# Optimization experiments

Hardware: AMD Instinct MI355X
Metric: run time of the kernel (lower is better)

## Reference

```python
import jax, jax.numpy as jnp
import numpy as np

N = 50000      # nodes
E = 800000     # edges (avg degree 16)
B = 128        # graphs in batch
F_IN = 30      # raw node feature dim
PORT_DIM = 32
FLAG_DIM = 2
H = 64         # hidden_dim; also F_IN+PORT_DIM+FLAG_DIM = 64
L = 3          # number of GraphConv layers
C = 10         # num_classes
TOTAL_PORTS = 65536
TCP_FLAGS_VALUES = 256


def setup_inputs() -> dict:
    key = jax.random.key(0)
    ks = jax.random.split(key, 20)
    s = 0.1  # weight init scale
    return {
        "x": jax.random.normal(ks[0], (N, F_IN), jnp.float32),
        "dst_ports": jax.random.randint(ks[1], (N,), 0, TOTAL_PORTS, jnp.int64),
        "tcp_flags": jax.random.randint(ks[2], (N,), 0, TCP_FLAGS_VALUES, jnp.int64),
        "edge_index": jax.random.randint(ks[3], (2, E), 0, N, jnp.int64),
        "batch": jnp.sort(jax.random.randint(ks[4], (N,), 0, B, jnp.int64)),
        # learned parameters
        "emb_port": jax.random.normal(ks[5], (TOTAL_PORTS, PORT_DIM), jnp.float32) * s,
        "emb_flags": jax.random.normal(ks[6], (TCP_FLAGS_VALUES, FLAG_DIM), jnp.float32) * s,
        "Wrel": jax.random.normal(ks[7], (L, H, H), jnp.float32) * s,   # lin_rel weight (out,in)
        "brel": jax.random.normal(ks[8], (L, H), jnp.float32) * s,      # lin_rel bias
        "Wroot": jax.random.normal(ks[9], (L, H, H), jnp.float32) * s,  # lin_root weight, no bias
        "fc1_W": jax.random.normal(ks[10], (H, H), jnp.float32) * s,
        "fc1_b": jax.random.normal(ks[11], (H,), jnp.float32) * s,
        "fc2_W": jax.random.normal(ks[12], (H, H), jnp.float32) * s,
        "fc2_b": jax.random.normal(ks[13], (H,), jnp.float32) * s,
        "fc3_W": jax.random.normal(ks[14], (C, H), jnp.float32) * s,
        "fc3_b": jax.random.normal(ks[15], (C,), jnp.float32) * s,
    }


def reference(x, dst_ports, tcp_flags, edge_index, batch,
              emb_port, emb_flags, Wrel, brel, Wroot,
              fc1_W, fc1_b, fc2_W, fc2_b, fc3_W, fc3_b):
    # embedding lookups + concat -> [N, 64]
    h = jnp.concatenate([x, emb_port[dst_ports], emb_flags[tcp_flags]], axis=1)
    src, dst = edge_index[0], edge_index[1]
    # PyG GraphConv (aggr='add'): h' = lin_rel(sum_{j->i} h_j) + lin_root(h_i)
    for l in range(L):
        agg = jax.ops.segment_sum(h[src], dst, num_segments=N)  # gather + scatter-add
        h = agg @ Wrel[l].T + brel[l] + h @ Wroot[l].T
        h = jax.nn.relu(h)  # dropout inactive (eval mode)
    # global_max_pool over graphs -> [B, H]
    g = jax.ops.segment_max(h, batch, num_segments=B)
    # MLP head (dropout inactive)
    g = jax.nn.relu(g @ fc1_W.T + fc1_b)
    g = jax.nn.relu(g @ fc2_W.T + fc2_b)
    return g @ fc3_W.T + fc3_b
```

## Files before the change

### kernel.cpp

```cpp
#include <hip/hip_runtime.h>

#define NN 50000
#define NE 800000
#define NB 128
#define FIN 30
#define H 64
#define NC 10
#define L 3

#define EBS 2048
#define NEB 391
#define NBX 391
#define NS (NBX * NEB)
#define SECAP 2816

typedef unsigned int uint;
typedef unsigned short ushort;
typedef __attribute__((ext_vector_type(8))) short bf16x8;
typedef __attribute__((ext_vector_type(4))) float f32x4;

__device__ __forceinline__ ushort f2bf(float x) {
    uint u = __float_as_uint(x);
    u += 0x7fffu + ((u >> 16) & 1u);
    return (ushort)(u >> 16);
}
__device__ __forceinline__ float bf_lo(uint v) { return __uint_as_float(v << 16); }
__device__ __forceinline__ float bf_hi(uint v) { return __uint_as_float(v & 0xffff0000u); }


__global__ __launch_bounds__(256) void prep_weights_kernel(
    const float* __restrict__ Wrel, const float* __restrict__ Wroot,
    ushort* __restrict__ Wb)
{
    int t = blockIdx.x * 256 + threadIdx.x;
    if (t >= L * 2 * H * H) return;
    int l = t / (2 * H * H), rem = t % (2 * H * H);
    int mat = rem / (H * H), jk = rem % (H * H);
    const float* W = mat ? Wroot : Wrel;
    Wb[t] = f2bf(W[l * H * H + jk]);
}

__global__ __launch_bounds__(256) void count_kernel(
    const int* __restrict__ dst, int* __restrict__ counts)
{
    __shared__ int cnt[NBX];
    int eb = blockIdx.x, tid = threadIdx.x;
    for (int t = tid; t < NBX; t += 256) cnt[t] = 0;
    __syncthreads();
#pragma unroll
    for (int q = 0; q < 8; ++q) {
        int e = eb * EBS + q * 256 + tid;
        if (e < NE) atomicAdd(&cnt[dst[e] >> 7], 1);
    }
    __syncthreads();
    for (int t = tid; t < NBX; t += 256) counts[t * NEB + eb] = cnt[t];
}

__global__ __launch_bounds__(1024) void scanA1_kernel(
    const int* __restrict__ counts, int* __restrict__ offs, int* __restrict__ bsum)
{
    __shared__ int wsum[16];
    int i = blockIdx.x * 1024 + threadIdx.x;
    int lane = threadIdx.x & 63;
    int wv = threadIdx.x >> 6;
    int v = (i < NS) ? counts[i] : 0;
    int s = v;
    for (int off = 1; off < 64; off <<= 1) {
        int t = __shfl_up(s, off);
        if (lane >= off) s += t;
    }
    if (lane == 63) wsum[wv] = s;
    __syncthreads();
    if (wv == 0) {
        int ws = (lane < 16) ? wsum[lane] : 0;
        for (int off = 1; off < 16; off <<= 1) {
            int t = __shfl_up(ws, off);
            if (lane >= off) ws += t;
        }
        if (lane < 16) wsum[lane] = ws;
    }
    __syncthreads();
    int base = (wv > 0) ? wsum[wv - 1] : 0;
    s += base;
    if (i < NS) offs[i] = s - v;
    if (threadIdx.x == 1023) bsum[blockIdx.x] = s;
}

__global__ __launch_bounds__(256) void scanA2_kernel(int* __restrict__ bsum, int nblk)
{
    __shared__ int arr[256];
    int t = threadIdx.x;
    int v = (t < nblk) ? bsum[t] : 0;
    arr[t] = v;
    __syncthreads();
    for (int off = 1; off < 256; off <<= 1) {
        int u = (t >= off) ? arr[t - off] : 0;
        __syncthreads();
        arr[t] += u;
        __syncthreads();
    }
    if (t < nblk) bsum[t] = arr[t] - v;
}

__global__ __launch_bounds__(1024) void scanA3_kernel(
    int* __restrict__ offs, const int* __restrict__ bsum)
{
    int b = blockIdx.x + 1;
    int i = b * 1024 + threadIdx.x;
    if (i < NS) offs[i] += bsum[b];
}

__global__ __launch_bounds__(256) void scatter_ranked_kernel(
    const int* __restrict__ src, const int* __restrict__ dst,
    const int* __restrict__ offs, int* __restrict__ tmp)
{
    __shared__ int cur[NBX];
    int eb = blockIdx.x, tid = threadIdx.x;
    for (int t = tid; t < NBX; t += 256) cur[t] = offs[t * NEB + eb];
    __syncthreads();
#pragma unroll
    for (int q = 0; q < 8; ++q) {
        int e = eb * EBS + q * 256 + tid;
        if (e < NE) {
            int d = dst[e];
            int b = d >> 7;
            int pos = atomicAdd(&cur[b], 1);
            tmp[pos] = (src[e] << 7) | (d & 127);
        }
    }
}

__global__ __launch_bounds__(256) void bucket_sort_kernel(
    const int* __restrict__ tmp, const int* __restrict__ offs,
    int* __restrict__ edge_arr, int2* __restrict__ node_range)
{
    __shared__ int se[SECAP];
    __shared__ int cnt[128];
    __shared__ int off[128];
    __shared__ int cur[128];
    int b = blockIdx.x, tid = threadIdx.x;
    int start = offs[b * NEB];
    int end   = (b + 1 < NBX) ? offs[(b + 1) * NEB] : NE;
    int ec = end - start; if (ec > SECAP) ec = SECAP;

    if (tid < 128) cnt[tid] = 0;
    __syncthreads();
    for (int t = tid; t < ec; t += 256) {
        int v = tmp[start + t];
        se[t] = v;
        atomicAdd(&cnt[v & 127], 1);
    }
    __syncthreads();
    if (tid < 64) {
        int v0 = cnt[2 * tid], v1 = cnt[2 * tid + 1];
        int s = v0 + v1;
        for (int o = 1; o < 64; o <<= 1) {
            int t = __shfl_up(s, o);
            if (tid >= o) s += t;
        }
        off[2 * tid]     = s - v1 - v0;
        off[2 * tid + 1] = s - v1;
        cur[2 * tid]     = s - v1 - v0;
        cur[2 * tid + 1] = s - v1;
    }
    __syncthreads();
    for (int t = tid; t < ec; t += 256) {
        int v = se[t];
        int p = atomicAdd(&cur[v & 127], 1);
        edge_arr[start + p] = v & ~127;
    }
    if (tid < 128) {
        int n = b * 128 + tid;
        if (n < NN) node_range[n] = make_int2(start + off[tid], cnt[tid]);
    }
}

__global__ __launch_bounds__(256) void gemm0_fused_kernel(
    const float* __restrict__ x, const int* __restrict__ ports,
    const int* __restrict__ flags, const float* __restrict__ emb_port,
    const float* __restrict__ emb_flags,
    const ushort* __restrict__ Wb, const float* __restrict__ brel,
    ushort* __restrict__ z0, ushort* __restrict__ z1)
{
    __shared__ float sf[64 * 65];
    __shared__ float so[64 * 65];
    int tid = threadIdx.x, lane = tid & 63, w = tid >> 6;
    int node0 = blockIdx.x * 64;

    for (int t = tid; t < 4096; t += 256) {
        int r = t >> 6, f = t & 63;
        int n = node0 + r;
        float v = 0.f;
        if (n < NN) {
            if (f < FIN)       v = x[(size_t)n * FIN + f];
            else if (f < 62)   v = emb_port[(size_t)ports[n] * 32 + (f - FIN)];
            else               v = emb_flags[(size_t)flags[n] * 2 + (f - 62)];
        }
        sf[r * 65 + f] = v;
    }
    __syncthreads();

    int m  = lane & 15;
    int kg = lane >> 4;
    int rloc = w * 16 + m;
    const float* fr = &sf[rloc * 65 + kg * 8];
    bf16x8 a0, a1;
#pragma unroll
    for (int i = 0; i < 8; ++i) {
        a0[i] = (short)f2bf(fr[i]);
        a1[i] = (short)f2bf(fr[32 + i]);
    }

    f32x4 acc0[4], acc1[4];
#pragma unroll
    for (int jt = 0; jt < 4; ++jt) {
        const ushort* wr0 = Wb + ((size_t)(jt * 16 + m)) * 64 + kg * 8;
        const ushort* wr1 = wr0 + (size_t)H * H;
        bf16x8 b00 = *(const bf16x8*)(wr0);
        bf16x8 b01 = *(const bf16x8*)(wr0 + 32);
        bf16x8 b10 = *(const bf16x8*)(wr1);
        bf16x8 b11 = *(const bf16x8*)(wr1 + 32);
        float bias = brel[jt * 16 + m];
        acc0[jt] = f32x4{0.f, 0.f, 0.f, 0.f};
        acc1[jt] = f32x4{bias, bias, bias, bias};
        acc0[jt] = __builtin_amdgcn_mfma_f32_16x16x32_bf16(a0, b00, acc0[jt], 0, 0, 0);
        acc0[jt] = __builtin_amdgcn_mfma_f32_16x16x32_bf16(a1, b01, acc0[jt], 0, 0, 0);
        acc1[jt] = __builtin_amdgcn_mfma_f32_16x16x32_bf16(a0, b10, acc1[jt], 0, 0, 0);
        acc1[jt] = __builtin_amdgcn_mfma_f32_16x16x32_bf16(a1, b11, acc1[jt], 0, 0, 0);
    }

    int nl = w * 16 + kg * 4;

#pragma unroll
    for (int jt = 0; jt < 4; ++jt)
#pragma unroll
        for (int r = 0; r < 4; ++r)
            so[(nl + r) * 65 + jt * 16 + m] = acc0[jt][r];
    __syncthreads();
    for (int t = tid; t < 512; t += 256) {
        int rr = t >> 3, oct = t & 7;
        if (node0 + rr < NN) {
            const float* s = &so[rr * 65 + oct * 8];
            uint4 v;
            v.x = (uint)f2bf(s[0]) | ((uint)f2bf(s[1]) << 16);
            v.y = (uint)f2bf(s[2]) | ((uint)f2bf(s[3]) << 16);
            v.z = (uint)f2bf(s[4]) | ((uint)f2bf(s[5]) << 16);
            v.w = (uint)f2bf(s[6]) | ((uint)f2bf(s[7]) << 16);
            *((uint4*)(z0 + (size_t)node0 * H) + t) = v;
        }
    }
    __syncthreads();

#pragma unroll
    for (int jt = 0; jt < 4; ++jt)
#pragma unroll
        for (int r = 0; r < 4; ++r)
            so[(nl + r) * 65 + jt * 16 + m] = acc1[jt][r];
    __syncthreads();
    for (int t = tid; t < 512; t += 256) {
        int rr = t >> 3, oct = t & 7;
        if (node0 + rr < NN) {
            const float* s = &so[rr * 65 + oct * 8];
            uint4 v;
            v.x = (uint)f2bf(s[0]) | ((uint)f2bf(s[1]) << 16);
            v.y = (uint)f2bf(s[2]) | ((uint)f2bf(s[3]) << 16);
            v.z = (uint)f2bf(s[4]) | ((uint)f2bf(s[5]) << 16);
            v.w = (uint)f2bf(s[6]) | ((uint)f2bf(s[7]) << 16);
            *((uint4*)(z1 + (size_t)node0 * H) + t) = v;
        }
    }
}

__global__ __launch_bounds__(256) void gemm_kernel(
    const ushort* __restrict__ h_in, const ushort* __restrict__ Wb,
    const float* __restrict__ brel,
    ushort* __restrict__ z0, ushort* __restrict__ z1)
{
    __shared__ float so[64 * 65];
    int tid = threadIdx.x, lane = tid & 63, w = tid >> 6;
    int m  = lane & 15;
    int kg = lane >> 4;
    int node0 = blockIdx.x * 64 + w * 16;

    int row = node0 + m; if (row >= NN) row = NN - 1;
    const ushort* hr = h_in + (size_t)row * H + kg * 8;
    bf16x8 a0 = *(const bf16x8*)(hr);
    bf16x8 a1 = *(const bf16x8*)(hr + 32);

    f32x4 acc0[4], acc1[4];
#pragma unroll
    for (int jt = 0; jt < 4; ++jt) {
        const ushort* wr0 = Wb + ((size_t)(jt * 16 + m)) * 64 + kg * 8;
        const ushort* wr1 = wr0 + (size_t)H * H;
        bf16x8 b00 = *(const bf16x8*)(wr0);
        bf16x8 b01 = *(const bf16x8*)(wr0 + 32);
        bf16x8 b10 = *(const bf16x8*)(wr1);
        bf16x8 b11 = *(const bf16x8*)(wr1 + 32);
        float bias = brel[jt * 16 + m];
        acc0[jt] = f32x4{0.f, 0.f, 0.f, 0.f};
        acc1[jt] = f32x4{bias, bias, bias, bias};
        acc0[jt] = __builtin_amdgcn_mfma_f32_16x16x32_bf16(a0, b00, acc0[jt], 0, 0, 0);
        acc0[jt] = __builtin_amdgcn_mfma_f32_16x16x32_bf16(a1, b01, acc0[jt], 0, 0, 0);
        acc1[jt] = __builtin_amdgcn_mfma_f32_16x16x32_bf16(a0, b10, acc1[jt], 0, 0, 0);
        acc1[jt] = __builtin_amdgcn_mfma_f32_16x16x32_bf16(a1, b11, acc1[jt], 0, 0, 0);
    }

    int nl = w * 16 + kg * 4;
    int nodeS0 = blockIdx.x * 64;

#pragma unroll
    for (int jt = 0; jt < 4; ++jt)
#pragma unroll
        for (int r = 0; r < 4; ++r)
            so[(nl + r) * 65 + jt * 16 + m] = acc0[jt][r];
    __syncthreads();
    for (int t = tid; t < 512; t += 256) {
        int rr = t >> 3, oct = t & 7;
        if (nodeS0 + rr < NN) {
            const float* s = &so[rr * 65 + oct * 8];
            uint4 v;
            v.x = (uint)f2bf(s[0]) | ((uint)f2bf(s[1]) << 16);
            v.y = (uint)f2bf(s[2]) | ((uint)f2bf(s[3]) << 16);
            v.z = (uint)f2bf(s[4]) | ((uint)f2bf(s[5]) << 16);
            v.w = (uint)f2bf(s[6]) | ((uint)f2bf(s[7]) << 16);
            *((uint4*)(z0 + (size_t)nodeS0 * H) + t) = v;
        }
    }
    __syncthreads();

#pragma unroll
    for (int jt = 0; jt < 4; ++jt)
#pragma unroll
        for (int r = 0; r < 4; ++r)
            so[(nl + r) * 65 + jt * 16 + m] = acc1[jt][r];
    __syncthreads();
    for (int t = tid; t < 512; t += 256) {
        int rr = t >> 3, oct = t & 7;
        if (nodeS0 + rr < NN) {
            const float* s = &so[rr * 65 + oct * 8];
            uint4 v;
            v.x = (uint)f2bf(s[0]) | ((uint)f2bf(s[1]) << 16);
            v.y = (uint)f2bf(s[2]) | ((uint)f2bf(s[3]) << 16);
            v.z = (uint)f2bf(s[4]) | ((uint)f2bf(s[5]) << 16);
            v.w = (uint)f2bf(s[6]) | ((uint)f2bf(s[7]) << 16);
            *((uint4*)(z1 + (size_t)nodeS0 * H) + t) = v;
        }
    }
}

__global__ __launch_bounds__(256) void gather_relu_kernel(
    const ushort* __restrict__ z0, const ushort* __restrict__ z1,
    const int2* __restrict__ node_range, const int* __restrict__ edge_arr,
    ushort* __restrict__ h_out)
{
    int tid = blockIdx.x * 256 + threadIdx.x;
    int n = tid >> 3, oct = tid & 7;
    if (n >= NN) return;
    int2 rng = node_range[n];
    int p0 = rng.x, p1 = rng.x + rng.y;
    const char* zb = (const char*)z0 + oct * 16;
    float a[8] = {0.f,0.f,0.f,0.f,0.f,0.f,0.f,0.f};
    for (int p = p0; p < p1; p += 8) {
        bool g[8]; int o[8]; uint4 v[8];
#pragma unroll
        for (int q = 0; q < 8; ++q) {
            g[q] = (p + q) < p1;
            o[q] = g[q] ? edge_arr[p + q] : 0;
        }
#pragma unroll
        for (int q = 0; q < 8; ++q) {
            v[q] = make_uint4(0u, 0u, 0u, 0u);
            if (g[q]) v[q] = *(const uint4*)(zb + o[q]);
        }
#pragma unroll
        for (int q = 0; q < 8; ++q) {
            a[0] += bf_lo(v[q].x); a[1] += bf_hi(v[q].x);
            a[2] += bf_lo(v[q].y); a[3] += bf_hi(v[q].y);
            a[4] += bf_lo(v[q].z); a[5] += bf_hi(v[q].z);
            a[6] += bf_lo(v[q].w); a[7] += bf_hi(v[q].w);
        }
    }
    uint4 sv = *(const uint4*)((const char*)z1 + (size_t)n * 128 + oct * 16);
    a[0] += bf_lo(sv.x); a[1] += bf_hi(sv.x);
    a[2] += bf_lo(sv.y); a[3] += bf_hi(sv.y);
    a[4] += bf_lo(sv.z); a[5] += bf_hi(sv.z);
    a[6] += bf_lo(sv.w); a[7] += bf_hi(sv.w);
    uint4 o;
    o.x = (uint)f2bf(fmaxf(a[0], 0.f)) | ((uint)f2bf(fmaxf(a[1], 0.f)) << 16);
    o.y = (uint)f2bf(fmaxf(a[2], 0.f)) | ((uint)f2bf(fmaxf(a[3], 0.f)) << 16);
    o.z = (uint)f2bf(fmaxf(a[4], 0.f)) | ((uint)f2bf(fmaxf(a[5], 0.f)) << 16);
    o.w = (uint)f2bf(fmaxf(a[6], 0.f)) | ((uint)f2bf(fmaxf(a[7], 0.f)) << 16);
    *((uint4*)h_out + tid) = o;
}

__global__ __launch_bounds__(256) void pool_mlp_kernel(
    const ushort* __restrict__ h, const int* __restrict__ batch,
    const float* __restrict__ fc1W, const float* __restrict__ fc1b,
    const float* __restrict__ fc2W, const float* __restrict__ fc2b,
    const float* __restrict__ fc3W, const float* __restrict__ fc3b,
    float* __restrict__ out)
{
    __shared__ float red[4][64];
    __shared__ float s0[64];
    __shared__ float s1[64];
    __shared__ float s2[64];
    int b = blockIdx.x;
    int tid = threadIdx.x;
    int f = tid & 63, w = tid >> 6;
    int lo = 0, hi = NN;
    while (lo < hi) { int mid = (lo + hi) >> 1; if (batch[mid] < b) lo = mid + 1; else hi = mid; }
    int lo2 = lo, hi2 = NN;
    while (lo2 < hi2) { int mid = (lo2 + hi2) >> 1; if (batch[mid] < b + 1) lo2 = mid + 1; else hi2 = mid; }
    float m = -3.402823466e38f;
    for (int n = lo + w; n < lo2; n += 4) {
        ushort u = h[(size_t)n * H + f];
        m = fmaxf(m, __uint_as_float((uint)u << 16));
    }
    red[w][f] = m;
    __syncthreads();
    int j = tid;
    if (tid < 64)
        s0[j] = fmaxf(fmaxf(red[0][j], red[1][j]), fmaxf(red[2][j], red[3][j]));
    __syncthreads();
    float acc = 0.f;
    if (tid < 64) {
        acc = fc1b[j];
        for (int k = 0; k < 64; ++k) acc = fmaf(s0[k], fc1W[j * 64 + k], acc);
    }
    __syncthreads();
    if (tid < 64) s1[j] = fmaxf(acc, 0.f);
    __syncthreads();
    if (tid < 64) {
        acc = fc2b[j];
        for (int k = 0; k < 64; ++k) acc = fmaf(s1[k], fc2W[j * 64 + k], acc);
    }
    __syncthreads();
    if (tid < 64) s2[j] = fmaxf(acc, 0.f);
    __syncthreads();
    if (tid < NC) {
        acc = fc3b[j];
        for (int k = 0; k < 64; ++k) acc = fmaf(s2[k], fc3W[j * 64 + k], acc);
        out[b * NC + j] = acc;
    }
}


extern "C" void kernel_launch(void* const* d_in, const int* in_sizes, int n_in,
                              void* d_out, int out_size, void* d_ws, size_t ws_size,
                              hipStream_t stream)
{
    const float* x         = (const float*)d_in[0];
    const int*   dst_ports = (const int*)d_in[1];
    const int*   tcp_flags = (const int*)d_in[2];
    const int*   edge_src_in = (const int*)d_in[3];
    const int*   edge_dst_in = edge_src_in + NE;
    const int*   batch     = (const int*)d_in[4];
    const float* emb_port  = (const float*)d_in[5];
    const float* emb_flags = (const float*)d_in[6];
    const float* Wrel      = (const float*)d_in[7];
    const float* brel      = (const float*)d_in[8];
    const float* Wroot     = (const float*)d_in[9];
    const float* fc1W      = (const float*)d_in[10];
    const float* fc1b      = (const float*)d_in[11];
    const float* fc2W      = (const float*)d_in[12];
    const float* fc2b      = (const float*)d_in[13];
    const float* fc3W      = (const float*)d_in[14];
    const float* fc3b      = (const float*)d_in[15];
    float* out = (float*)d_out;

    char* ws = (char*)d_ws;
    size_t off = 0;
    auto alloc = [&](size_t bytes) {
        void* p = ws + off;
        off += (bytes + 255) & ~(size_t)255;
        return p;
    };
    ushort* hA        = (ushort*)alloc((size_t)NN * H * 2);
    ushort* hB        = (ushort*)alloc((size_t)NN * H * 2);
    ushort* z0        = (ushort*)alloc((size_t)NN * H * 2);
    ushort* z1        = (ushort*)alloc((size_t)NN * H * 2);
    int*    counts    = (int*)alloc((size_t)NS * 4);
    int*    tmp       = (int*)alloc((size_t)NE * 4);
    int*    edge_arr  = (int*)alloc((size_t)NE * 4);
    int2*   node_range= (int2*)alloc((size_t)NN * 8);
    int*    bsum      = (int*)alloc((size_t)256 * 4);
    ushort* Wb        = (ushort*)alloc((size_t)L * 2 * H * H * 2);

    const int SBLK = (NS + 1023) / 1024;

    prep_weights_kernel<<<96, 256, 0, stream>>>(Wrel, Wroot, Wb);

    count_kernel<<<NEB, 256, 0, stream>>>(edge_dst_in, counts);
    scanA1_kernel<<<SBLK, 1024, 0, stream>>>(counts, counts, bsum);
    scanA2_kernel<<<1, 256, 0, stream>>>(bsum, SBLK);
    scanA3_kernel<<<SBLK - 1, 1024, 0, stream>>>(counts, bsum);
    scatter_ranked_kernel<<<NEB, 256, 0, stream>>>(edge_src_in, edge_dst_in, counts, tmp);
    bucket_sort_kernel<<<NBX, 256, 0, stream>>>(tmp, counts, edge_arr, node_range);

    const int ggrid = (NN + 63) / 64;
    const int agrid = (NN * 8 + 255) / 256;
    gemm0_fused_kernel<<<ggrid, 256, 0, stream>>>(
        x, dst_ports, tcp_flags, emb_port, emb_flags, Wb, brel, z0, z1);
    gather_relu_kernel<<<agrid, 256, 0, stream>>>(z0, z1, node_range, edge_arr, hA);

    gemm_kernel<<<ggrid, 256, 0, stream>>>(
        hA, Wb + (size_t)1 * 2 * H * H, brel + 1 * H, z0, z1);
    gather_relu_kernel<<<agrid, 256, 0, stream>>>(z0, z1, node_range, edge_arr, hB);
    gemm_kernel<<<ggrid, 256, 0, stream>>>(
        hB, Wb + (size_t)2 * 2 * H * H, brel + 2 * H, z0, z1);
    gather_relu_kernel<<<agrid, 256, 0, stream>>>(z0, z1, node_range, edge_arr, hA);

    pool_mlp_kernel<<<NB, 256, 0, stream>>>(
        hA, batch, fc1W, fc1b, fc2W, fc2b, fc3W, fc3b, out);
}
```

Measured before the change: 272.3 us.

## Merge setup kernels, pad edge lists to remove gather guards, widen pooling

Folds weight conversion into the count kernel and the edge scatter into the first GEMM launch, so fewer kernels launch and independent work shares one grid. Per-node edge lists are padded to multiples of eight with a pointer to a zeroed sentinel row, which lets the gather loop drop its bounds checks. Pooling now uses 512 threads per graph. The padding adds edge array memory and extra sentinel loads, and the fused launches rely on block-index splitting.

New measurement: 243.2 us. -10.7%, faster.

```diff
diff --git a/kernel.cpp b/kernel.cpp
--- a/kernel.cpp
+++ b/kernel.cpp
@@ -13,6 +13,8 @@
 #define NBX 391
 #define NS (NBX * NEB)
 #define SECAP 2816
+#define PCAP 3456
+#define ZOFF (NN << 7)
 
 typedef unsigned int uint;
 typedef unsigned short ushort;
@@ -28,32 +30,34 @@
 __device__ __forceinline__ float bf_hi(uint v) { return __uint_as_float(v & 0xffff0000u); }
 
 
-__global__ __launch_bounds__(256) void prep_weights_kernel(
+__global__ __launch_bounds__(256) void count_prep_kernel(
+    const int* __restrict__ dst, int* __restrict__ counts,
     const float* __restrict__ Wrel, const float* __restrict__ Wroot,
-    ushort* __restrict__ Wb)
-{
-    int t = blockIdx.x * 256 + threadIdx.x;
-    if (t >= L * 2 * H * H) return;
-    int l = t / (2 * H * H), rem = t % (2 * H * H);
-    int mat = rem / (H * H), jk = rem % (H * H);
-    const float* W = mat ? Wroot : Wrel;
-    Wb[t] = f2bf(W[l * H * H + jk]);
-}
-
-__global__ __launch_bounds__(256) void count_kernel(
-    const int* __restrict__ dst, int* __restrict__ counts)
+    ushort* __restrict__ Wb, ushort* __restrict__ z0)
 {
     __shared__ int cnt[NBX];
-    int eb = blockIdx.x, tid = threadIdx.x;
-    for (int t = tid; t < NBX; t += 256) cnt[t] = 0;
-    __syncthreads();
-#pragma unroll
-    for (int q = 0; q < 8; ++q) {
-        int e = eb * EBS + q * 256 + tid;
-        if (e < NE) atomicAdd(&cnt[dst[e] >> 7], 1);
-    }
-    __syncthreads();
-    for (int t = tid; t < NBX; t += 256) counts[t * NEB + eb] = cnt[t];
+    int bid = blockIdx.x, tid = threadIdx.x;
+    if (bid < NEB) {
+        for (int t = tid; t < NBX; t += 256) cnt[t] = 0;
+        __syncthreads();
+#pragma unroll
+        for (int q = 0; q < 8; ++q) {
+            int e = bid * EBS + q * 256 + tid;
+            if (e < NE) atomicAdd(&cnt[dst[e] >> 7], 1);
+        }
+        __syncthreads();
+        for (int t = tid; t < NBX; t += 256) counts[t * NEB + bid] = cnt[t];
+    } else if (bid < NEB + 96) {
+        int t = (bid - NEB) * 256 + tid;
+        if (t < L * 2 * H * H) {
+            int l = t / (2 * H * H), rem = t % (2 * H * H);
+            int mat = rem / (H * H), jk = rem % (H * H);
+            const float* W = mat ? Wroot : Wrel;
+            Wb[t] = f2bf(W[l * H * H + jk]);
+        }
+    } else {
+        if (tid < 8) ((uint4*)(z0 + (size_t)NN * H))[tid] = make_uint4(0u, 0u, 0u, 0u);
+    }
 }
 
 __global__ __launch_bounds__(1024) void scanA1_kernel(
@@ -110,72 +114,9 @@
     if (i < NS) offs[i] += bsum[b];
 }
 
-__global__ __launch_bounds__(256) void scatter_ranked_kernel(
-    const int* __restrict__ src, const int* __restrict__ dst,
-    const int* __restrict__ offs, int* __restrict__ tmp)
-{
-    __shared__ int cur[NBX];
-    int eb = blockIdx.x, tid = threadIdx.x;
-    for (int t = tid; t < NBX; t += 256) cur[t] = offs[t * NEB + eb];
-    __syncthreads();
-#pragma unroll
-    for (int q = 0; q < 8; ++q) {
-        int e = eb * EBS + q * 256 + tid;
-        if (e < NE) {
-            int d = dst[e];
-            int b = d >> 7;
-            int pos = atomicAdd(&cur[b], 1);
-            tmp[pos] = (src[e] << 7) | (d & 127);
-        }
-    }
-}
-
-__global__ __launch_bounds__(256) void bucket_sort_kernel(
-    const int* __restrict__ tmp, const int* __restrict__ offs,
-    int* __restrict__ edge_arr, int2* __restrict__ node_range)
-{
-    __shared__ int se[SECAP];
-    __shared__ int cnt[128];
-    __shared__ int off[128];
-    __shared__ int cur[128];
-    int b = blockIdx.x, tid = threadIdx.x;
-    int start = offs[b * NEB];
-    int end   = (b + 1 < NBX) ? offs[(b + 1) * NEB] : NE;
-    int ec = end - start; if (ec > SECAP) ec = SECAP;
-
-    if (tid < 128) cnt[tid] = 0;
-    __syncthreads();
-    for (int t = tid; t < ec; t += 256) {
-        int v = tmp[start + t];
-        se[t] = v;
-        atomicAdd(&cnt[v & 127], 1);
-    }
-    __syncthreads();
-    if (tid < 64) {
-        int v0 = cnt[2 * tid], v1 = cnt[2 * tid + 1];
-        int s = v0 + v1;
-        for (int o = 1; o < 64; o <<= 1) {
-            int t = __shfl_up(s, o);
-            if (tid >= o) s += t;
-        }
-        off[2 * tid]     = s - v1 - v0;
-        off[2 * tid + 1] = s - v1;
-        cur[2 * tid]     = s - v1 - v0;
-        cur[2 * tid + 1] = s - v1;
-    }
-    __syncthreads();
-    for (int t = tid; t < ec; t += 256) {
-        int v = se[t];
-        int p = atomicAdd(&cur[v & 127], 1);
-        edge_arr[start + p] = v & ~127;
-    }
-    if (tid < 128) {
-        int n = b * 128 + tid;
-        if (n < NN) node_range[n] = make_int2(start + off[tid], cnt[tid]);
-    }
-}
-
-__global__ __launch_bounds__(256) void gemm0_fused_kernel(
+__global__ __launch_bounds__(256) void scatter_gemm0_kernel(
+    const int* __restrict__ srcv, const int* __restrict__ dstv,
+    const int* __restrict__ offs, int* __restrict__ tmp,
     const float* __restrict__ x, const int* __restrict__ ports,
     const int* __restrict__ flags, const float* __restrict__ emb_port,
     const float* __restrict__ emb_flags,
@@ -184,8 +125,28 @@
 {
     __shared__ float sf[64 * 65];
     __shared__ float so[64 * 65];
-    int tid = threadIdx.x, lane = tid & 63, w = tid >> 6;
-    int node0 = blockIdx.x * 64;
+    __shared__ int cur[NBX];
+    int bid = blockIdx.x, tid = threadIdx.x;
+
+    if (bid < NEB) {
+        for (int t = tid; t < NBX; t += 256) cur[t] = offs[t * NEB + bid];
+        __syncthreads();
+#pragma unroll
+        for (int q = 0; q < 8; ++q) {
+            int e = bid * EBS + q * 256 + tid;
+            if (e < NE) {
+                int d = dstv[e];
+                int b = d >> 7;
+                int pos = atomicAdd(&cur[b], 1);
+                tmp[pos] = (srcv[e] << 7) | (d & 127);
+            }
+        }
+        return;
+    }
+
+    int gb = bid - NEB;
+    int lane = tid & 63, w = tid >> 6;
+    int node0 = gb * 64;
 
     for (int t = tid; t < 4096; t += 256) {
         int r = t >> 6, f = t & 63;
@@ -271,6 +232,58 @@
     }
 }
 
+__global__ __launch_bounds__(256) void bucket_sort_kernel(
+    const int* __restrict__ tmp, const int* __restrict__ offs,
+    int* __restrict__ edge_arr, int2* __restrict__ node_range)
+{
+    __shared__ int se[SECAP];
+    __shared__ int cnt[128];
+    __shared__ int po[128];
+    __shared__ int cur[128];
+    int b = blockIdx.x, tid = threadIdx.x;
+    int start = offs[b * NEB];
+    int end   = (b + 1 < NBX) ? offs[(b + 1) * NEB] : NE;
+    int ec = end - start; if (ec > SECAP) ec = SECAP;
+
+    if (tid < 128) cnt[tid] = 0;
+    __syncthreads();
+    for (int t = tid; t < ec; t += 256) {
+        int v = tmp[start + t];
+        se[t] = v;
+        atomicAdd(&cnt[v & 127], 1);
+    }
+    __syncthreads();
+    if (tid < 64) {
+        int c0 = cnt[2 * tid], c1 = cnt[2 * tid + 1];
+        int p0 = (c0 + 7) & ~7, p1 = (c1 + 7) & ~7;
+        int s = p0 + p1;
+        for (int o = 1; o < 64; o <<= 1) {
+            int t = __shfl_up(s, o);
+            if (tid >= o) s += t;
+        }
+        po[2 * tid]     = s - p1 - p0;
+        po[2 * tid + 1] = s - p1;
+        cur[2 * tid]     = s - p1 - p0;
+        cur[2 * tid + 1] = s - p1;
+    }
+    __syncthreads();
+    int base = b * PCAP;
+    for (int t = tid; t < ec; t += 256) {
+        int v = se[t];
+        int p = atomicAdd(&cur[v & 127], 1);
+        edge_arr[base + p] = v & ~127;
+    }
+    __syncthreads();
+    if (tid < 128) {
+        int c = cnt[tid];
+        int pd = (c + 7) & ~7;
+        for (int q = c; q < pd; ++q)
+            edge_arr[base + po[tid] + q] = ZOFF;
+        int n = b * 128 + tid;
+        if (n < NN) node_range[n] = make_int2(base + po[tid], c);
+    }
+}
+
 __global__ __launch_bounds__(256) void gemm_kernel(
     const ushort* __restrict__ h_in, const ushort* __restrict__ Wb,
     const float* __restrict__ brel,
@@ -357,20 +370,16 @@
     int n = tid >> 3, oct = tid & 7;
     if (n >= NN) return;
     int2 rng = node_range[n];
-    int p0 = rng.x, p1 = rng.x + rng.y;
+    int p0 = rng.x;
+    int pend = p0 + ((rng.y + 7) & ~7);
     const char* zb = (const char*)z0 + oct * 16;
     float a[8] = {0.f,0.f,0.f,0.f,0.f,0.f,0.f,0.f};
-    for (int p = p0; p < p1; p += 8) {
-        bool g[8]; int o[8]; uint4 v[8];
+    for (int p = p0; p < pend; p += 8) {
+        uint4 v[8];
 #pragma unroll
         for (int q = 0; q < 8; ++q) {
-            g[q] = (p + q) < p1;
-            o[q] = g[q] ? edge_arr[p + q] : 0;
-        }
-#pragma unroll
-        for (int q = 0; q < 8; ++q) {
-            v[q] = make_uint4(0u, 0u, 0u, 0u);
-            if (g[q]) v[q] = *(const uint4*)(zb + o[q]);
+            int o = edge_arr[p + q];
+            v[q] = *(const uint4*)(zb + o);
         }
 #pragma unroll
         for (int q = 0; q < 8; ++q) {
@@ -393,14 +402,14 @@
     *((uint4*)h_out + tid) = o;
 }
 
-__global__ __launch_bounds__(256) void pool_mlp_kernel(
+__global__ __launch_bounds__(512) void pool_mlp_kernel(
     const ushort* __restrict__ h, const int* __restrict__ batch,
     const float* __restrict__ fc1W, const float* __restrict__ fc1b,
     const float* __restrict__ fc2W, const float* __restrict__ fc2b,
     const float* __restrict__ fc3W, const float* __restrict__ fc3b,
     float* __restrict__ out)
 {
-    __shared__ float red[4][64];
+    __shared__ float red[8][64];
     __shared__ float s0[64];
     __shared__ float s1[64];
     __shared__ float s2[64];
@@ -412,15 +421,19 @@
     int lo2 = lo, hi2 = NN;
     while (lo2 < hi2) { int mid = (lo2 + hi2) >> 1; if (batch[mid] < b + 1) lo2 = mid + 1; else hi2 = mid; }
     float m = -3.402823466e38f;
-    for (int n = lo + w; n < lo2; n += 4) {
+    for (int n = lo + w; n < lo2; n += 8) {
         ushort u = h[(size_t)n * H + f];
         m = fmaxf(m, __uint_as_float((uint)u << 16));
     }
     red[w][f] = m;
     __syncthreads();
     int j = tid;
-    if (tid < 64)
-        s0[j] = fmaxf(fmaxf(red[0][j], red[1][j]), fmaxf(red[2][j], red[3][j]));
+    if (tid < 64) {
+        float mm = red[0][j];
+#pragma unroll
+        for (int q = 1; q < 8; ++q) mm = fmaxf(mm, red[q][j]);
+        s0[j] = mm;
+    }
     __syncthreads();
     float acc = 0.f;
     if (tid < 64) {
@@ -477,30 +490,32 @@
     };
     ushort* hA        = (ushort*)alloc((size_t)NN * H * 2);
     ushort* hB        = (ushort*)alloc((size_t)NN * H * 2);
-    ushort* z0        = (ushort*)alloc((size_t)NN * H * 2);
+    ushort* z0        = (ushort*)alloc((size_t)(NN + 1) * H * 2);
     ushort* z1        = (ushort*)alloc((size_t)NN * H * 2);
     int*    counts    = (int*)alloc((size_t)NS * 4);
     int*    tmp       = (int*)alloc((size_t)NE * 4);
-    int*    edge_arr  = (int*)alloc((size_t)NE * 4);
+    int*    edge_arr  = (int*)alloc((size_t)NBX * PCAP * 4);
     int2*   node_range= (int2*)alloc((size_t)NN * 8);
     int*    bsum      = (int*)alloc((size_t)256 * 4);
     ushort* Wb        = (ushort*)alloc((size_t)L * 2 * H * H * 2);
 
     const int SBLK = (NS + 1023) / 1024;
 
-    prep_weights_kernel<<<96, 256, 0, stream>>>(Wrel, Wroot, Wb);
-
-    count_kernel<<<NEB, 256, 0, stream>>>(edge_dst_in, counts);
+    count_prep_kernel<<<NEB + 96 + 1, 256, 0, stream>>>(
+        edge_dst_in, counts, Wrel, Wroot, Wb, z0);
+
     scanA1_kernel<<<SBLK, 1024, 0, stream>>>(counts, counts, bsum);
     scanA2_kernel<<<1, 256, 0, stream>>>(bsum, SBLK);
     scanA3_kernel<<<SBLK - 1, 1024, 0, stream>>>(counts, bsum);
-    scatter_ranked_kernel<<<NEB, 256, 0, stream>>>(edge_src_in, edge_dst_in, counts, tmp);
+
+    const int ggrid = (NN + 63) / 64;
+    scatter_gemm0_kernel<<<NEB + ggrid, 256, 0, stream>>>(
+        edge_src_in, edge_dst_in, counts, tmp,
+        x, dst_ports, tcp_flags, emb_port, emb_flags, Wb, brel, z0, z1);
+
     bucket_sort_kernel<<<NBX, 256, 0, stream>>>(tmp, counts, edge_arr, node_range);
 
-    const int ggrid = (NN + 63) / 64;
     const int agrid = (NN * 8 + 255) / 256;
-    gemm0_fused_kernel<<<ggrid, 256, 0, stream>>>(
-        x, dst_ports, tcp_flags, emb_port, emb_flags, Wb, brel, z0, z1);
     gather_relu_kernel<<<agrid, 256, 0, stream>>>(z0, z1, node_range, edge_arr, hA);
 
     gemm_kernel<<<ggrid, 256, 0, stream>>>(
@@ -510,6 +525,6 @@
         hB, Wb + (size_t)2 * 2 * H * H, brel + 2 * H, z0, z1);
     gather_relu_kernel<<<agrid, 256, 0, stream>>>(z0, z1, node_range, edge_arr, hA);
 
-    pool_mlp_kernel<<<NB, 256, 0, stream>>>(
+    pool_mlp_kernel<<<NB, 512, 0, stream>>>(
         hA, batch, fc1W, fc1b, fc2W, fc2b, fc3W, fc3b, out);
 }
```
